# Performance work log

Hardware: AMD Instinct MI355X
Metric: run time of the kernel (lower is better)

## Reference

```python
import jax, jax.numpy as jnp
import numpy as np

N_HEAD = 16

def setup_inputs() -> dict:
    key = jax.random.key(0)
    k1, k2, k3 = jax.random.split(key, 3)
    B, T, D = 2, 2048, 1024
    x = jax.random.normal(k1, (B, T, D), dtype=jnp.float32)
    sigma_qkv = float(np.sqrt(2.0 / (D + 3 * D)))
    sigma_out = float(np.sqrt(2.0 / (D + D)))
    W_qkv = jax.random.truncated_normal(k2, -3.0, 3.0, (3 * D, D), dtype=jnp.float32) * sigma_qkv
    W_out = jax.random.truncated_normal(k3, -3.0, 3.0, (D, D), dtype=jnp.float32) * sigma_out
    return {"x": x, "W_qkv": W_qkv, "W_out": W_out}


def reference(x, W_qkv, W_out):
    B, T, C = x.shape
    H = N_HEAD
    hd = C // H
    qkv = x @ W_qkv.T  # (B,T,3C)
    q, k, v = jnp.split(qkv, 3, axis=-1)
    # (B,T,C) -> (B,H,T,hd)
    q = q.reshape(B, T, H, hd).transpose(0, 2, 1, 3)
    k = k.reshape(B, T, H, hd).transpose(0, 2, 1, 3)
    v = v.reshape(B, T, H, hd).transpose(0, 2, 1, 3)
    scale = 1.0 / jnp.sqrt(jnp.asarray(hd, dtype=x.dtype))
    score = jnp.einsum('bhqd,bhkd->bhqk', q, k) * scale  # (B,H,T,T)
    causal = jnp.tril(jnp.ones((T, T), dtype=bool))
    score = jnp.where(causal, score, -jnp.inf)
    attn = jax.nn.softmax(score, axis=-1)
    out = jnp.einsum('bhqk,bhkd->bhqd', attn, v)  # (B,H,T,hd)
    out = out.transpose(0, 2, 1, 3).reshape(B, T, C)
    return out @ W_out.T
```

## Files before the change

### kernel.cpp

```cpp
#include <hip/hip_runtime.h>
#include <hip/hip_bf16.h>
#include <cstdint>

typedef unsigned short u16;
typedef __attribute__((ext_vector_type(8))) short bf16x8;
typedef __attribute__((ext_vector_type(4))) float f32x4;

#define T_SEQ 2048
#define NHEAD 16
#define HDIM  64
#define NB    2

__device__ __forceinline__ float bf2f(uint32_t h) { return __uint_as_float(h << 16); }
__device__ __forceinline__ u16 f2bf(float f) {
    uint32_t u = __float_as_uint(f);
    u += 0x7fffu + ((u >> 16) & 1u);
    return (u16)(u >> 16);
}

__device__ __forceinline__ void gl_lds16(const u16* g, u16* s) {
    __builtin_amdgcn_global_load_lds(
        (const __attribute__((address_space(1))) unsigned int*)g,
        (__attribute__((address_space(3))) unsigned int*)s, 16, 0, 0);
}

__global__ void detect_dtype(const uint32_t* __restrict__ x, int* __restrict__ flag) {
    __shared__ int red[4];
    int c = 0;
#pragma unroll
    for (int j = 0; j < 4; j++) {
        uint32_t v = x[threadIdx.x * 4 + j];
        uint32_t lo = v & 0xffffu;
        uint32_t e = (lo >> 7) & 0xffu;
        if (lo != 0u && e >= 110u && e <= 135u) c++;
    }
#pragma unroll
    for (int off = 32; off; off >>= 1) c += __shfl_down(c, off);
    if ((threadIdx.x & 63) == 0) red[threadIdx.x >> 6] = c;
    __syncthreads();
    if (threadIdx.x == 0)
        *flag = (red[0] + red[1] + red[2] + red[3] > 614) ? 1 : 0;
}

__global__ __launch_bounds__(256) void to_bf16(
    const void* __restrict__ src, u16* __restrict__ dst, int n4,
    const int* __restrict__ flag)
{
    int i = blockIdx.x * 256 + threadIdx.x;
    const int stride = gridDim.x * 256;
    if (*flag != 0) {
        const uint2* s = (const uint2*)src;
        uint2* d = (uint2*)dst;
        for (; i < n4; i += stride) d[i] = s[i];
    } else {
        const float4* s = (const float4*)src;
        for (; i < n4; i += stride) {
            float4 v = s[i];
            ushort4 o = { f2bf(v.x), f2bf(v.y), f2bf(v.z), f2bf(v.w) };
            *(ushort4*)(dst + (size_t)i * 4) = o;
        }
    }
}

template<int BM, int MODE>
__global__ __launch_bounds__(256, 3) void gemm_bt_mfma(
    const u16* __restrict__ A, const u16* __restrict__ B,
    int N, int K,
    u16* __restrict__ qo, u16* __restrict__ ko, u16* __restrict__ vt,
    u16* __restrict__ outb16, float* __restrict__ outf32,
    const int* __restrict__ flag)
{
    constexpr int WM = BM / 2;
    constexpr int MI = WM / 16;
    constexpr int IA = BM / 32;
    constexpr int ST = 2 * BM * 64 * 2;
    constexpr int E16 = 4 * WM * 72 * 2;
    constexpr int EF = (MODE == 1) ? 4 * WM * (WM + 4) * 4 : 0;
    constexpr int SB = (ST > E16 ? ST : E16) > EF ? (ST > E16 ? ST : E16) : EF;
    __shared__ u16 smem[SB / 2];
    u16* As = smem;
    u16* Bs = smem + BM * 64;
    const int tid = threadIdx.x;
    const int bm = blockIdx.y * BM, bn = blockIdx.x * BM;
    const int w = tid >> 6, lane = tid & 63;
    const int wm = (w >> 1) * WM, wn = (w & 1) * WM;
    const int n16 = lane & 15, quad = lane >> 4;
    const int l8 = lane >> 3, c8 = lane & 7;

    f32x4 acc[MI][MI];
#pragma unroll
    for (int mi = 0; mi < MI; mi++)
#pragma unroll
        for (int ni = 0; ni < MI; ni++) acc[mi][ni] = (f32x4){0.f, 0.f, 0.f, 0.f};

    const int KT = K >> 6;
    for (int kt = 0; kt < KT; kt++) {
        const int k0 = kt << 6;
#pragma unroll
        for (int i = 0; i < IA; i++) {
            int rowblk = (i * 4 + w) * 8;
            int row = rowblk + l8;
            int gcol = (c8 ^ l8) * 8;
            gl_lds16(A + (size_t)(bm + row) * K + k0 + gcol, As + rowblk * 64);
            gl_lds16(B + (size_t)(bn + row) * K + k0 + gcol, Bs + rowblk * 64);
        }
        __syncthreads();
#pragma unroll
        for (int ks = 0; ks < 2; ks++) {
            bf16x8 af[MI], bfr[MI];
#pragma unroll
            for (int mi = 0; mi < MI; mi++) {
                int row = wm + mi * 16 + n16;
                af[mi] = *(const bf16x8*)(As + row * 64 + (((ks * 4 + quad) ^ (n16 & 7)) * 8));
            }
#pragma unroll
            for (int ni = 0; ni < MI; ni++) {
                int row = wn + ni * 16 + n16;
                bfr[ni] = *(const bf16x8*)(Bs + row * 64 + (((ks * 4 + quad) ^ (n16 & 7)) * 8));
            }
#pragma unroll
            for (int mi = 0; mi < MI; mi++)
#pragma unroll
                for (int ni = 0; ni < MI; ni++)
                    acc[mi][ni] = __builtin_amdgcn_mfma_f32_16x16x32_bf16(
                        af[mi], bfr[ni], acc[mi][ni], 0, 0, 0);
        }
        __syncthreads();
    }

    if constexpr (MODE == 0) {
        u16* ep = smem + w * (WM * 72);
        const int which = (bn + wn) >> 10;
        const int hq = ((bn + wn) & 1023) >> 6;
        const int bb = (bm + wm) >> 11;
        const int tb = (bm + wm) & (T_SEQ - 1);
        if (which == 2) {
#pragma unroll
            for (int mi = 0; mi < MI; mi++)
#pragma unroll
                for (int ni = 0; ni < MI; ni++)
#pragma unroll
                    for (int r = 0; r < 4; r++)
                        ep[(ni * 16 + n16) * 72 + mi * 16 + quad * 4 + r] = f2bf(acc[mi][ni][r]);
            asm volatile("s_waitcnt lgkmcnt(0)" ::: "memory");
            u16* dst = vt + ((size_t)(bb * NHEAD + hq) * HDIM) * T_SEQ + tb;
#pragma unroll
            for (int it = 0; it < 8; it++) {
                int row = it * 8 + l8, col = c8 * 8;
                bf16x8 v = *(const bf16x8*)(ep + row * 72 + col);
                *(bf16x8*)(dst + (size_t)row * T_SEQ + col) = v;
            }
        } else {
            const float sc = which ? 1.f : 0.125f;
#pragma unroll
            for (int mi = 0; mi < MI; mi++)
#pragma unroll
                for (int ni = 0; ni < MI; ni++)
#pragma unroll
                    for (int r = 0; r < 4; r++)
                        ep[(mi * 16 + quad * 4 + r) * 72 + ni * 16 + n16] = f2bf(acc[mi][ni][r] * sc);
            asm volatile("s_waitcnt lgkmcnt(0)" ::: "memory");
            u16* dst = (which ? ko : qo) + ((size_t)(bb * NHEAD + hq) * T_SEQ + tb) * HDIM;
#pragma unroll
            for (int it = 0; it < 8; it++) {
                int row = it * 8 + l8, col = c8 * 8;
                bf16x8 v = *(const bf16x8*)(ep + row * 72 + col);
                *(bf16x8*)(dst + (size_t)row * HDIM + col) = v;
            }
        }
    } else {
        if (*flag == 0) {
            float* epf = (float*)smem + w * (WM * (WM + 4));
#pragma unroll
            for (int mi = 0; mi < MI; mi++)
#pragma unroll
                for (int ni = 0; ni < MI; ni++)
#pragma unroll
                    for (int r = 0; r < 4; r++)
                        epf[(mi * 16 + quad * 4 + r) * (WM + 4) + ni * 16 + n16] = acc[mi][ni][r];
            asm volatile("s_waitcnt lgkmcnt(0)" ::: "memory");
            constexpr int LPR = WM / 4;
            constexpr int RPI = 64 / LPR;
#pragma unroll
            for (int it = 0; it < WM / RPI; it++) {
                int row = it * RPI + lane / LPR, col = (lane % LPR) * 4;
                float4 v = *(const float4*)(epf + row * (WM + 4) + col);
                *(float4*)(outf32 + (size_t)(bm + wm + row) * N + bn + wn + col) = v;
            }
        } else {
            u16* ep = smem + w * (WM * 72);
#pragma unroll
            for (int mi = 0; mi < MI; mi++)
#pragma unroll
                for (int ni = 0; ni < MI; ni++)
#pragma unroll
                    for (int r = 0; r < 4; r++)
                        ep[(mi * 16 + quad * 4 + r) * 72 + ni * 16 + n16] = f2bf(acc[mi][ni][r]);
            asm volatile("s_waitcnt lgkmcnt(0)" ::: "memory");
            constexpr int LPR = WM / 8;
            constexpr int RPI = 64 / LPR;
#pragma unroll
            for (int it = 0; it < WM / RPI; it++) {
                int row = it * RPI + lane / LPR, col = (lane % LPR) * 8;
                bf16x8 v = *(const bf16x8*)(ep + row * 72 + col);
                *(bf16x8*)(outb16 + (size_t)(bm + wm + row) * N + bn + wn + col) = v;
            }
        }
    }
}

__global__ __launch_bounds__(256, 2) void attn_mfma(
    const u16* __restrict__ qb, const u16* __restrict__ kb,
    const u16* __restrict__ vt, u16* __restrict__ ob)
{
    __shared__ u16 Ks[64 * 64];
    __shared__ u16 Vs[64 * 64];
    __shared__ u16 Plds[4][16][72];
    const int lin = blockIdx.x;
    const int xcd = lin & 7;
    const int rest = lin >> 3;
    const int p = rest & 15;
    const int grp = rest >> 4;
    const int bh = grp * 8 + xcd;
    const int qtb = 31 - p, qts = p;
    const int w = threadIdx.x >> 6, lane = threadIdx.x & 63;
    const int n16 = lane & 15, quad = lane >> 4;
    const int l8 = lane >> 3, c8 = lane & 7;
    const size_t baseK = (size_t)bh * T_SEQ * HDIM;
    const size_t baseV = (size_t)bh * HDIM * T_SEQ;
    const int b = bh >> 4, h = bh & 15;

    bf16x8 ones;
#pragma unroll
    for (int j = 0; j < 8; j++) ones[j] = (short)0x3F80;

    auto stage = [&](int kt) {
#pragma unroll
        for (int i = 0; i < 2; i++) {
            int rowblk = (i * 4 + w) * 8;
            int row = rowblk + l8;
            int gc = (c8 ^ l8) * 8;
            gl_lds16(kb + baseK + (size_t)(kt * 64 + row) * HDIM + gc, Ks + rowblk * 64);
            gl_lds16(vt + baseV + (size_t)row * T_SEQ + kt * 64 + gc, Vs + rowblk * 64);
        }
    };

    const int qrowb = qtb * 64 + w * 16, qrows = qts * 64 + w * 16;
    bf16x8 qfb[2], qfs[2];
#pragma unroll
    for (int ks = 0; ks < 2; ks++) {
        qfb[ks] = *(const bf16x8*)(qb + baseK + (size_t)(qrowb + n16) * HDIM + ks * 32 + quad * 8);
        qfs[ks] = *(const bf16x8*)(qb + baseK + (size_t)(qrows + n16) * HDIM + ks * 32 + quad * 8);
    }

    f32x4 accOb[4], accOs[4];
#pragma unroll
    for (int st = 0; st < 4; st++) {
        accOb[st] = (f32x4){0.f, 0.f, 0.f, 0.f};
        accOs[st] = (f32x4){0.f, 0.f, 0.f, 0.f};
    }
    f32x4 accLb = (f32x4){0.f, 0.f, 0.f, 0.f};
    f32x4 accLs = (f32x4){0.f, 0.f, 0.f, 0.f};

    stage(0);
    for (int kt = 0; kt <= qtb; kt++) {
        __syncthreads();

        bf16x8 kf[2][4], vf[2][4];
#pragma unroll
        for (int st = 0; st < 4; st++)
#pragma unroll
            for (int ks = 0; ks < 2; ks++) {
                int off = (st * 16 + n16) * 64 + (((ks * 4 + quad) ^ (n16 & 7)) * 8);
                kf[ks][st] = *(const bf16x8*)(Ks + off);
                vf[ks][st] = *(const bf16x8*)(Vs + off);
            }
        __syncthreads();

        if (kt < qtb) stage(kt + 1);

        {
            f32x4 S[4];
#pragma unroll
            for (int st = 0; st < 4; st++) S[st] = (f32x4){0.f, 0.f, 0.f, 0.f};
#pragma unroll
            for (int st = 0; st < 4; st++)
#pragma unroll
                for (int ks = 0; ks < 2; ks++)
                    S[st] = __builtin_amdgcn_mfma_f32_16x16x32_bf16(qfb[ks], kf[ks][st], S[st], 0, 0, 0);
            if (kt == qtb) {
                int qloc = w * 16 + quad * 4;
#pragma unroll
                for (int st = 0; st < 4; st++) {
                    int kloc = st * 16 + n16;
#pragma unroll
                    for (int r = 0; r < 4; r++)
                        if (kloc > qloc + r) S[st][r] = -INFINITY;
                }
            }
#pragma unroll
            for (int st = 0; st < 4; st++)
#pragma unroll
                for (int r = 0; r < 4; r++) {
                    float pv = exp2f(__builtin_fmaf(S[st][r], 1.44269504f, -14.4269504f));
                    Plds[w][quad * 4 + r][st * 16 + n16] = (u16)(__float_as_uint(pv) >> 16);
                }
            asm volatile("s_waitcnt lgkmcnt(0)" ::: "memory");
            bf16x8 pf[2];
#pragma unroll
            for (int ks = 0; ks < 2; ks++)
                pf[ks] = *(const bf16x8*)(&Plds[w][n16][ks * 32 + quad * 8]);
#pragma unroll
            for (int st = 0; st < 4; st++)
#pragma unroll
                for (int ks = 0; ks < 2; ks++)
                    accOb[st] = __builtin_amdgcn_mfma_f32_16x16x32_bf16(pf[ks], vf[ks][st], accOb[st], 0, 0, 0);
#pragma unroll
            for (int ks = 0; ks < 2; ks++)
                accLb = __builtin_amdgcn_mfma_f32_16x16x32_bf16(pf[ks], ones, accLb, 0, 0, 0);
        }

        if (kt <= qts) {
            f32x4 S[4];
#pragma unroll
            for (int st = 0; st < 4; st++) S[st] = (f32x4){0.f, 0.f, 0.f, 0.f};
#pragma unroll
            for (int st = 0; st < 4; st++)
#pragma unroll
                for (int ks = 0; ks < 2; ks++)
                    S[st] = __builtin_amdgcn_mfma_f32_16x16x32_bf16(qfs[ks], kf[ks][st], S[st], 0, 0, 0);
            if (kt == qts) {
                int qloc = w * 16 + quad * 4;
#pragma unroll
                for (int st = 0; st < 4; st++) {
                    int kloc = st * 16 + n16;
#pragma unroll
                    for (int r = 0; r < 4; r++)
                        if (kloc > qloc + r) S[st][r] = -INFINITY;
                }
            }
#pragma unroll
            for (int st = 0; st < 4; st++)
#pragma unroll
                for (int r = 0; r < 4; r++) {
                    float pv = exp2f(__builtin_fmaf(S[st][r], 1.44269504f, -14.4269504f));
                    Plds[w][quad * 4 + r][st * 16 + n16] = (u16)(__float_as_uint(pv) >> 16);
                }
            asm volatile("s_waitcnt lgkmcnt(0)" ::: "memory");
            bf16x8 pf[2];
#pragma unroll
            for (int ks = 0; ks < 2; ks++)
                pf[ks] = *(const bf16x8*)(&Plds[w][n16][ks * 32 + quad * 8]);
#pragma unroll
            for (int st = 0; st < 4; st++)
#pragma unroll
                for (int ks = 0; ks < 2; ks++)
                    accOs[st] = __builtin_amdgcn_mfma_f32_16x16x32_bf16(pf[ks], vf[ks][st], accOs[st], 0, 0, 0);
#pragma unroll
            for (int ks = 0; ks < 2; ks++)
                accLs = __builtin_amdgcn_mfma_f32_16x16x32_bf16(pf[ks], ones, accLs, 0, 0, 0);
        }
    }

#pragma unroll
    for (int r = 0; r < 4; r++) {
        float inv = 1.f / accLb[r];
#pragma unroll
        for (int st = 0; st < 4; st++)
            Plds[w][quad * 4 + r][st * 16 + n16] = f2bf(accOb[st][r] * inv);
    }
    asm volatile("s_waitcnt lgkmcnt(0)" ::: "memory");
    u16* dstb = ob + ((size_t)(b * T_SEQ + qrowb)) * 1024 + h * HDIM;
#pragma unroll
    for (int it = 0; it < 2; it++) {
        int row = it * 8 + l8, col = c8 * 8;
        bf16x8 v = *(const bf16x8*)(&Plds[w][row][col]);
        *(bf16x8*)(dstb + (size_t)row * 1024 + col) = v;
    }
    asm volatile("s_waitcnt lgkmcnt(0)" ::: "memory");
#pragma unroll
    for (int r = 0; r < 4; r++) {
        float inv = 1.f / accLs[r];
#pragma unroll
        for (int st = 0; st < 4; st++)
            Plds[w][quad * 4 + r][st * 16 + n16] = f2bf(accOs[st][r] * inv);
    }
    asm volatile("s_waitcnt lgkmcnt(0)" ::: "memory");
    u16* dsts = ob + ((size_t)(b * T_SEQ + qrows)) * 1024 + h * HDIM;
#pragma unroll
    for (int it = 0; it < 2; it++) {
        int row = it * 8 + l8, col = c8 * 8;
        bf16x8 v = *(const bf16x8*)(&Plds[w][row][col]);
        *(bf16x8*)(dsts + (size_t)row * 1024 + col) = v;
    }
}

extern "C" void kernel_launch(void* const* d_in, const int* in_sizes, int n_in,
                              void* d_out, int out_size, void* d_ws, size_t ws_size,
                              hipStream_t stream) {
    const void* x    = d_in[0];
    const void* Wqkv = d_in[1];
    const void* Wout = d_in[2];

    const int Mtok = NB * T_SEQ;
    const size_t n_x    = (size_t)Mtok * 1024;
    const size_t n_wqkv = (size_t)3072 * 1024;
    const size_t n_wout = (size_t)1024 * 1024;
    const size_t qkv_elems = (size_t)NB * NHEAD * T_SEQ * HDIM;

    u16* xb    = (u16*)d_ws;
    u16* wqkvb = xb + n_x;
    u16* woutb = wqkvb + n_wqkv;
    u16* qb    = woutb + n_wout;
    u16* kb    = qb + qkv_elems;
    u16* vt    = kb + qkv_elems;
    u16* obuf  = vt + qkv_elems;
    int* flag  = (int*)(obuf + qkv_elems);

    detect_dtype<<<1, 256, 0, stream>>>((const uint32_t*)x, flag);

    to_bf16<<<1024, 256, 0, stream>>>(x,    xb,    (int)(n_x / 4),    flag);
    to_bf16<<<1024, 256, 0, stream>>>(Wqkv, wqkvb, (int)(n_wqkv / 4), flag);
    to_bf16<<<512,  256, 0, stream>>>(Wout, woutb, (int)(n_wout / 4), flag);

    gemm_bt_mfma<128, 0><<<dim3(3072 / 128, Mtok / 128), 256, 0, stream>>>(
        xb, wqkvb, 3072, 1024, qb, kb, vt, nullptr, nullptr, flag);

    attn_mfma<<<dim3(NB * NHEAD * (T_SEQ / 128)), 256, 0, stream>>>(qb, kb, vt, obuf);

    gemm_bt_mfma<64, 1><<<dim3(1024 / 64, Mtok / 64), 256, 0, stream>>>(
        obuf, woutb, 1024, 1024, nullptr, nullptr, nullptr,
        (u16*)d_out, (float*)d_out, flag);
}
```

Baseline: 169.5 us.

## Restructure causal attention into 8-wave blocks over contiguous 128-row query tiles

New measurement: 171.1 us. No clear change (+0.9%).

```diff
diff --git a/kernel.cpp b/kernel.cpp
--- a/kernel.cpp
+++ b/kernel.cpp
@@ -209,77 +209,72 @@
     }
 }
 
-__global__ __launch_bounds__(256, 2) void attn_mfma(
+__global__ __launch_bounds__(512, 4) void attn_mfma(
     const u16* __restrict__ qb, const u16* __restrict__ kb,
     const u16* __restrict__ vt, u16* __restrict__ ob)
 {
     __shared__ u16 Ks[64 * 64];
     __shared__ u16 Vs[64 * 64];
-    __shared__ u16 Plds[4][16][72];
-    const int lin = blockIdx.x;
-    const int xcd = lin & 7;
-    const int rest = lin >> 3;
-    const int p = rest & 15;
-    const int grp = rest >> 4;
-    const int bh = grp * 8 + xcd;
-    const int qtb = 31 - p, qts = p;
+    __shared__ u16 Plds[8][16][72];
+    const int bidx = blockIdx.x;
+    const int c = bidx & 255;
+    const int rr = bidx >> 8;
+    const int bh = c & 31;
+    const int jm = c >> 5;
+    const int t = rr ? (15 - jm) : jm;
     const int w = threadIdx.x >> 6, lane = threadIdx.x & 63;
     const int n16 = lane & 15, quad = lane >> 4;
     const int l8 = lane >> 3, c8 = lane & 7;
     const size_t baseK = (size_t)bh * T_SEQ * HDIM;
     const size_t baseV = (size_t)bh * HDIM * T_SEQ;
-    const int b = bh >> 4, h = bh & 15;
+    const int b = bh >> 4, head = bh & 15;
 
     bf16x8 ones;
 #pragma unroll
-    for (int j = 0; j < 8; j++) ones[j] = (short)0x3F80;
+    for (int e = 0; e < 8; e++) ones[e] = (short)0x3F80;
 
     auto stage = [&](int kt) {
-#pragma unroll
-        for (int i = 0; i < 2; i++) {
-            int rowblk = (i * 4 + w) * 8;
-            int row = rowblk + l8;
-            int gc = (c8 ^ l8) * 8;
-            gl_lds16(kb + baseK + (size_t)(kt * 64 + row) * HDIM + gc, Ks + rowblk * 64);
-            gl_lds16(vt + baseV + (size_t)row * T_SEQ + kt * 64 + gc, Vs + rowblk * 64);
-        }
+        int row = w * 8 + l8;
+        int gc = (c8 ^ l8) * 8;
+        gl_lds16(kb + baseK + (size_t)(kt * 64 + row) * HDIM + gc, Ks + (w * 8) * 64);
+        gl_lds16(vt + baseV + (size_t)row * T_SEQ + (size_t)kt * 64 + gc, Vs + (w * 8) * 64);
     };
 
-    const int qrowb = qtb * 64 + w * 16, qrows = qts * 64 + w * 16;
-    bf16x8 qfb[2], qfs[2];
-#pragma unroll
-    for (int ks = 0; ks < 2; ks++) {
-        qfb[ks] = *(const bf16x8*)(qb + baseK + (size_t)(qrowb + n16) * HDIM + ks * 32 + quad * 8);
-        qfs[ks] = *(const bf16x8*)(qb + baseK + (size_t)(qrows + n16) * HDIM + ks * 32 + quad * 8);
-    }
-
-    f32x4 accOb[4], accOs[4];
-#pragma unroll
-    for (int st = 0; st < 4; st++) {
-        accOb[st] = (f32x4){0.f, 0.f, 0.f, 0.f};
-        accOs[st] = (f32x4){0.f, 0.f, 0.f, 0.f};
-    }
-    f32x4 accLb = (f32x4){0.f, 0.f, 0.f, 0.f};
-    f32x4 accLs = (f32x4){0.f, 0.f, 0.f, 0.f};
+    const int qrow = t * 128 + w * 16;
+    bf16x8 qf[2];
+#pragma unroll
+    for (int ks = 0; ks < 2; ks++)
+        qf[ks] = *(const bf16x8*)(qb + baseK + (size_t)(qrow + n16) * HDIM + ks * 32 + quad * 8);
+
+    f32x4 accO[4];
+#pragma unroll
+    for (int st = 0; st < 4; st++) accO[st] = (f32x4){0.f, 0.f, 0.f, 0.f};
+    f32x4 accL = (f32x4){0.f, 0.f, 0.f, 0.f};
+
+    const int ktmax = 2 * t + 1;
+    const int kend  = 2 * t + (w >> 2);
 
     stage(0);
-    for (int kt = 0; kt <= qtb; kt++) {
+    for (int kt = 0; kt <= ktmax; kt++) {
         __syncthreads();
 
+        const bool act = (kt <= kend);
         bf16x8 kf[2][4], vf[2][4];
-#pragma unroll
-        for (int st = 0; st < 4; st++)
-#pragma unroll
-            for (int ks = 0; ks < 2; ks++) {
-                int off = (st * 16 + n16) * 64 + (((ks * 4 + quad) ^ (n16 & 7)) * 8);
-                kf[ks][st] = *(const bf16x8*)(Ks + off);
-                vf[ks][st] = *(const bf16x8*)(Vs + off);
-            }
+        if (act) {
+#pragma unroll
+            for (int st = 0; st < 4; st++)
+#pragma unroll
+                for (int ks = 0; ks < 2; ks++) {
+                    int off = (st * 16 + n16) * 64 + (((ks * 4 + quad) ^ (n16 & 7)) * 8);
+                    kf[ks][st] = *(const bf16x8*)(Ks + off);
+                    vf[ks][st] = *(const bf16x8*)(Vs + off);
+                }
+        }
         __syncthreads();
 
-        if (kt < qtb) stage(kt + 1);
-
-        {
+        if (kt < ktmax) stage(kt + 1);
+
+        if (act) {
             f32x4 S[4];
 #pragma unroll
             for (int st = 0; st < 4; st++) S[st] = (f32x4){0.f, 0.f, 0.f, 0.f};
@@ -287,9 +282,9 @@
             for (int st = 0; st < 4; st++)
 #pragma unroll
                 for (int ks = 0; ks < 2; ks++)
-                    S[st] = __builtin_amdgcn_mfma_f32_16x16x32_bf16(qfb[ks], kf[ks][st], S[st], 0, 0, 0);
-            if (kt == qtb) {
-                int qloc = w * 16 + quad * 4;
+                    S[st] = __builtin_amdgcn_mfma_f32_16x16x32_bf16(qf[ks], kf[ks][st], S[st], 0, 0, 0);
+            if (kt == kend) {
+                int qloc = (w & 3) * 16 + quad * 4;
 #pragma unroll
                 for (int st = 0; st < 4; st++) {
                     int kloc = st * 16 + n16;
@@ -314,84 +309,27 @@
             for (int st = 0; st < 4; st++)
 #pragma unroll
                 for (int ks = 0; ks < 2; ks++)
-                    accOb[st] = __builtin_amdgcn_mfma_f32_16x16x32_bf16(pf[ks], vf[ks][st], accOb[st], 0, 0, 0);
+                    accO[st] = __builtin_amdgcn_mfma_f32_16x16x32_bf16(pf[ks], vf[ks][st], accO[st], 0, 0, 0);
 #pragma unroll
             for (int ks = 0; ks < 2; ks++)
-                accLb = __builtin_amdgcn_mfma_f32_16x16x32_bf16(pf[ks], ones, accLb, 0, 0, 0);
-        }
-
-        if (kt <= qts) {
-            f32x4 S[4];
-#pragma unroll
-            for (int st = 0; st < 4; st++) S[st] = (f32x4){0.f, 0.f, 0.f, 0.f};
-#pragma unroll
-            for (int st = 0; st < 4; st++)
-#pragma unroll
-                for (int ks = 0; ks < 2; ks++)
-                    S[st] = __builtin_amdgcn_mfma_f32_16x16x32_bf16(qfs[ks], kf[ks][st], S[st], 0, 0, 0);
-            if (kt == qts) {
-                int qloc = w * 16 + quad * 4;
-#pragma unroll
-                for (int st = 0; st < 4; st++) {
-                    int kloc = st * 16 + n16;
-#pragma unroll
-                    for (int r = 0; r < 4; r++)
-                        if (kloc > qloc + r) S[st][r] = -INFINITY;
-                }
-            }
-#pragma unroll
-            for (int st = 0; st < 4; st++)
-#pragma unroll
-                for (int r = 0; r < 4; r++) {
-                    float pv = exp2f(__builtin_fmaf(S[st][r], 1.44269504f, -14.4269504f));
-                    Plds[w][quad * 4 + r][st * 16 + n16] = (u16)(__float_as_uint(pv) >> 16);
-                }
-            asm volatile("s_waitcnt lgkmcnt(0)" ::: "memory");
-            bf16x8 pf[2];
-#pragma unroll
-            for (int ks = 0; ks < 2; ks++)
-                pf[ks] = *(const bf16x8*)(&Plds[w][n16][ks * 32 + quad * 8]);
-#pragma unroll
-            for (int st = 0; st < 4; st++)
-#pragma unroll
-                for (int ks = 0; ks < 2; ks++)
-                    accOs[st] = __builtin_amdgcn_mfma_f32_16x16x32_bf16(pf[ks], vf[ks][st], accOs[st], 0, 0, 0);
-#pragma unroll
-            for (int ks = 0; ks < 2; ks++)
-                accLs = __builtin_amdgcn_mfma_f32_16x16x32_bf16(pf[ks], ones, accLs, 0, 0, 0);
+                accL = __builtin_amdgcn_mfma_f32_16x16x32_bf16(pf[ks], ones, accL, 0, 0, 0);
         }
     }
 
 #pragma unroll
     for (int r = 0; r < 4; r++) {
-        float inv = 1.f / accLb[r];
+        float inv = 1.f / accL[r];
 #pragma unroll
         for (int st = 0; st < 4; st++)
-            Plds[w][quad * 4 + r][st * 16 + n16] = f2bf(accOb[st][r] * inv);
+            Plds[w][quad * 4 + r][st * 16 + n16] = f2bf(accO[st][r] * inv);
     }
     asm volatile("s_waitcnt lgkmcnt(0)" ::: "memory");
-    u16* dstb = ob + ((size_t)(b * T_SEQ + qrowb)) * 1024 + h * HDIM;
+    u16* dst = ob + ((size_t)(b * T_SEQ + qrow)) * 1024 + head * HDIM;
 #pragma unroll
     for (int it = 0; it < 2; it++) {
         int row = it * 8 + l8, col = c8 * 8;
         bf16x8 v = *(const bf16x8*)(&Plds[w][row][col]);
-        *(bf16x8*)(dstb + (size_t)row * 1024 + col) = v;
-    }
-    asm volatile("s_waitcnt lgkmcnt(0)" ::: "memory");
-#pragma unroll
-    for (int r = 0; r < 4; r++) {
-        float inv = 1.f / accLs[r];
-#pragma unroll
-        for (int st = 0; st < 4; st++)
-            Plds[w][quad * 4 + r][st * 16 + n16] = f2bf(accOs[st][r] * inv);
-    }
-    asm volatile("s_waitcnt lgkmcnt(0)" ::: "memory");
-    u16* dsts = ob + ((size_t)(b * T_SEQ + qrows)) * 1024 + h * HDIM;
-#pragma unroll
-    for (int it = 0; it < 2; it++) {
-        int row = it * 8 + l8, col = c8 * 8;
-        bf16x8 v = *(const bf16x8*)(&Plds[w][row][col]);
-        *(bf16x8*)(dsts + (size_t)row * 1024 + col) = v;
+        *(bf16x8*)(dst + (size_t)row * 1024 + col) = v;
     }
 }
 
@@ -426,7 +364,7 @@
     gemm_bt_mfma<128, 0><<<dim3(3072 / 128, Mtok / 128), 256, 0, stream>>>(
         xb, wqkvb, 3072, 1024, qb, kb, vt, nullptr, nullptr, flag);
 
-    attn_mfma<<<dim3(NB * NHEAD * (T_SEQ / 128)), 256, 0, stream>>>(qb, kb, vt, obuf);
+    attn_mfma<<<dim3(NB * NHEAD * (T_SEQ / 128)), 512, 0, stream>>>(qb, kb, vt, obuf);
 
     gemm_bt_mfma<64, 1><<<dim3(1024 / 64, Mtok / 64), 256, 0, stream>>>(
         obuf, woutb, 1024, 1024, nullptr, nullptr, nullptr,
```
